# Kernel tuning notes

Hardware: AMD Instinct MI355X
Metric: run time of the kernel (lower is better)

The kernel has to match this reference:

```python
import jax, jax.numpy as jnp
import numpy as np

IMG, P, INC = 384, 2, 3
C = 2 * IMG            # embed_dim = 768
NP_ = IMG // P         # 192 patches
N = NP_ + 1            # 193 tokens with cls
L, H, E, K, B = 6, 12, 8, 2, 32
HD = C // H
EPS = 1e-5


def layer_norm(x, w, b):
    m = jnp.mean(x, -1, keepdims=True)
    v = jnp.mean((x - m) ** 2, -1, keepdims=True)
    return (x - m) * jax.lax.rsqrt(v + EPS) * w + b


def setup_inputs() -> dict:
    key = jax.random.key(0)
    ks = iter(jax.random.split(key, 32))
    nrm = lambda sh, s=0.02: jax.random.normal(next(ks), sh, jnp.float32) * s
    inp = {
        'x1': nrm((B, INC, IMG, IMG), 1.0),
        'x2': nrm((B, INC, IMG, IMG), 1.0),
        'patch_w': nrm((C, INC, IMG, P)),
        'patch_b': jnp.zeros((C,)),
        'cls_token': nrm((1, 1, C), 1e-6),
        'ln1_w': jnp.ones((L, C)), 'ln1_b': jnp.zeros((L, C)),
        'qkv_w': nrm((L, 3 * C, C)), 'qkv_b': jnp.zeros((L, 3 * C)),
        'proj_w': nrm((L, C, C)), 'proj_b': jnp.zeros((L, C)),
        'ln2_w': jnp.ones((L, C)), 'ln2_b': jnp.zeros((L, C)),
        'route_w': nrm((L, E, C)), 'route_b': jnp.zeros((L, E)),
        'rln_w': jnp.ones((L, E)), 'rln_b': jnp.zeros((L, E)),
        'expert_w': nrm((L, E, C, C)), 'expert_b': jnp.zeros((L, E, C)),
        'norm_w': jnp.ones((C,)), 'norm_b': jnp.zeros((C,)),
    }
    # fixed 1D sin-cos positional embedding (build_sincos_encoding)
    pd = C // 2
    omega = jnp.exp(jnp.arange(pd, dtype=jnp.float32) * (-np.log(10000.0) / pd))
    ow = jnp.arange(NP_, dtype=jnp.float32)[:, None] * omega
    pe = jnp.concatenate([jnp.sin(ow), jnp.cos(ow)], axis=1)          # [192, C]
    inp['pos_emb'] = jnp.concatenate([jnp.zeros((1, C)), pe], axis=0)[None]  # [1, N, C]
    return inp


def _patch_embed(x, patch_w, patch_b, cls_token, pos_emb):
    b = x.shape[0]
    # non-overlapping (IMG, P) conv == matmul on patches, flattened in (c, kh, kw) order
    xp = x.reshape(b, INC, IMG, NP_, P).transpose(0, 3, 1, 2, 4).reshape(b, NP_, INC * IMG * P)
    tok = xp @ patch_w.reshape(C, -1).T + patch_b                     # [B, 192, C]
    tok = jnp.concatenate([jnp.broadcast_to(cls_token, (b, 1, C)), tok], axis=1)
    return tok + pos_emb


def _encoder(x, view_id, ln1_w, ln1_b, qkv_w, qkv_b, proj_w, proj_b,
             ln2_w, ln2_b, route_w, route_b, rln_w, rln_b, expert_w, expert_b):
    scale = HD ** -0.5
    base = jax.random.fold_in(jax.random.key(1234), view_id)
    b = x.shape[0]

    def step(h, p):
        idx, l1w, l1b, qw, qb, pw, pb, l2w, l2b, rw, rb, rlw, rlb, ew, eb = p
        # --- attention ---
        y = layer_norm(h, l1w, l1b)
        qkv = (y @ qw.T + qb).reshape(b, N, 3, H, HD).transpose(2, 0, 3, 1, 4)
        q, k, v = qkv[0], qkv[1], qkv[2]
        a = jax.nn.softmax(jnp.einsum('bhqd,bhkd->bhqk', q, k) * scale, axis=-1)
        o = jnp.einsum('bhqk,bhkd->bhqd', a, v).transpose(0, 2, 1, 3).reshape(b, N, C)
        h = h + o @ pw.T + pb
        # --- MoE ---
        y = layer_norm(h, l2w, l2b)
        logits = layer_norm(y @ rw.T + rb, rlw, rlb)                  # [B, N, E]
        noise = jax.random.normal(jax.random.fold_in(base, idx), logits.shape) / E
        rwts = jax.nn.softmax(logits, axis=-1) + noise
        topw, topi = jax.lax.top_k(rwts, K)
        topw = jax.nn.softmax(topw, axis=-1)
        # dense all-expert compute, as in the source module
        eo = jnp.einsum('bni,eoi->bneo', y, ew) + eb                  # [B, N, E, C]
        sel = jnp.take_along_axis(eo, topi[..., None], axis=2)        # [B, N, K, C]
        h = h + (sel * topw[..., None]).sum(axis=2)
        return h, None

    xs = (jnp.arange(L), ln1_w, ln1_b, qkv_w, qkv_b, proj_w, proj_b,
          ln2_w, ln2_b, route_w, route_b, rln_w, rln_b, expert_w, expert_b)
    x, _ = jax.lax.scan(step, x, xs)
    return x


def reference(x1, x2, patch_w, patch_b, cls_token, ln1_w, ln1_b, qkv_w, qkv_b,
              proj_w, proj_b, ln2_w, ln2_b, route_w, route_b, rln_w, rln_b,
              expert_w, expert_b, norm_w, norm_b, pos_emb):
    def tower(x, vid):
        h = _patch_embed(x, patch_w, patch_b, cls_token, pos_emb)
        h = _encoder(h, vid, ln1_w, ln1_b, qkv_w, qkv_b, proj_w, proj_b,
                     ln2_w, ln2_b, route_w, route_b, rln_w, rln_b, expert_w, expert_b)
        return layer_norm(h, norm_w, norm_b)[:, 0]
    return jnp.concatenate([tower(x1, 0), tower(x2, 1)], axis=1)      # [B, 2*C]
```

## Files before the change

kernel.cpp:

```cpp
#include <hip/hip_runtime.h>
#include <stdint.h>

#define C_DIM   768
#define N_TOK   193
#define B_TOT   64
#define ROWS    (B_TOT * N_TOK)
#define QKV_DIM 2304
#define N_HEAD  12
#define N_EXP   8
#define MAXPER  ROWS
#define RTOK    64

enum { MODE_PATCH = 0, MODE_PLAIN = 1, MODE_RESID = 2, MODE_EXPERT = 3 };

typedef __attribute__((ext_vector_type(8))) short bf16x8;
typedef __attribute__((ext_vector_type(4))) float f32x4;

__device__ __forceinline__ uint32_t rotl32(uint32_t x, int n){ return (x << n) | (x >> (32 - n)); }

__device__ __forceinline__ void tf2x32(uint32_t k0, uint32_t k1, uint32_t x0, uint32_t x1,
                                       uint32_t &r0, uint32_t &r1){
  uint32_t k2 = k0 ^ k1 ^ 0x1BD11BDAu;
#define TF4(a,b,c,d) x0+=x1; x1=rotl32(x1,a); x1^=x0; x0+=x1; x1=rotl32(x1,b); x1^=x0; \
                     x0+=x1; x1=rotl32(x1,c); x1^=x0; x0+=x1; x1=rotl32(x1,d); x1^=x0;
  x0 += k0; x1 += k1;
  TF4(13,15,26, 6)  x0 += k1; x1 += k2 + 1u;
  TF4(17,29,16,24)  x0 += k2; x1 += k0 + 2u;
  TF4(13,15,26, 6)  x0 += k0; x1 += k1 + 3u;
  TF4(17,29,16,24)  x0 += k1; x1 += k2 + 4u;
  TF4(13,15,26, 6)  x0 += k2; x1 += k0 + 5u;
#undef TF4
  r0 = x0; r1 = x1;
}

__device__ __forceinline__ float jax_erfinv(float x){
  float w = -log1pf(-x * x);
  float p;
  if (w < 5.0f){
    w -= 2.5f;
    p =              2.81022636e-08f;
    p = fmaf(p, w,   3.43273939e-07f);
    p = fmaf(p, w,  -3.5233877e-06f);
    p = fmaf(p, w,  -4.39150654e-06f);
    p = fmaf(p, w,   0.00021858087f);
    p = fmaf(p, w,  -0.00125372503f);
    p = fmaf(p, w,  -0.00417768164f);
    p = fmaf(p, w,   0.246640727f);
    p = fmaf(p, w,   1.50140941f);
  } else {
    w = sqrtf(w) - 3.0f;
    p =             -0.000200214257f;
    p = fmaf(p, w,   0.000100950558f);
    p = fmaf(p, w,   0.00134934322f);
    p = fmaf(p, w,  -0.00367342844f);
    p = fmaf(p, w,   0.00573950773f);
    p = fmaf(p, w,  -0.0076224613f);
    p = fmaf(p, w,   0.00943887047f);
    p = fmaf(p, w,   1.00167406f);
    p = fmaf(p, w,   2.83297682f);
  }
  return p * x;
}

__device__ __forceinline__ float jax_noise(uint32_t c0, uint32_t c1, uint32_t j){
  uint32_t o0, o1;
  tf2x32(c0, c1, 0u, j, o0, o1);
  uint32_t bits = o0 ^ o1;
  float f = __uint_as_float(0x3f800000u | (bits >> 9)) - 1.0f;
  const float lo = -0.99999994f;
  float u = fmaxf(lo, f * 2.0f + lo);
  return 1.41421356237f * jax_erfinv(u) * 0.125f;
}

__device__ __forceinline__ unsigned short f2bf(float x){
  union { float f; uint32_t u; } v; v.f = x;
  uint32_t u = v.u;
  uint32_t r = (u + 0x7FFFu + ((u >> 16) & 1u)) >> 16;
  return (unsigned short)r;
}
__device__ __forceinline__ float bf2f(unsigned short h){
  union { uint32_t u; float f; } v; v.u = ((uint32_t)h) << 16;
  return v.f;
}

__global__ __launch_bounds__(64) void k_zero8(int* __restrict__ p){
  if ((int)threadIdx.x < N_EXP) p[threadIdx.x] = 0;
}

__global__ __launch_bounds__(64) void k_sentinel(float* __restrict__ out, float v){
  if (threadIdx.x == 0) out[0] = v;
}

__global__ __launch_bounds__(256) void k_cls(float* __restrict__ h, const float* __restrict__ cls,
                                             const float* __restrict__ pos){
  const int bt = blockIdx.x;
  #pragma unroll
  for (int u = 0; u < 3; ++u){
    int c = threadIdx.x + u * 256;
    h[(size_t)bt * N_TOK * C_DIM + c] = cls[c] + pos[c];
  }
}

__device__ __forceinline__ float blk_sum(float v, float* sb){
  #pragma unroll
  for (int off = 32; off > 0; off >>= 1) v += __shfl_down(v, off, 64);
  const int lane = threadIdx.x & 63, w = threadIdx.x >> 6;
  if (lane == 0) sb[w] = v;
  __syncthreads();
  if (threadIdx.x == 0) sb[4] = sb[0] + sb[1] + sb[2] + sb[3];
  __syncthreads();
  float r = sb[4];
  __syncthreads();
  return r;
}

__global__ __launch_bounds__(256) void k_layernorm(const float* __restrict__ x, float* __restrict__ y,
                                                   const float* __restrict__ w, const float* __restrict__ b){
  __shared__ float sb[8];
  const float* xr = x + (size_t)blockIdx.x * C_DIM;
  float v0 = xr[threadIdx.x], v1 = xr[threadIdx.x + 256], v2 = xr[threadIdx.x + 512];
  float mean = blk_sum(v0 + v1 + v2, sb) * (1.0f / 768.0f);
  float d0 = v0 - mean, d1 = v1 - mean, d2 = v2 - mean;
  float var = blk_sum(d0 * d0 + d1 * d1 + d2 * d2, sb) * (1.0f / 768.0f);
  float inv = 1.0f / sqrtf(var + 1e-5f);
  float* yr = y + (size_t)blockIdx.x * C_DIM;
  yr[threadIdx.x]       = d0 * inv * w[threadIdx.x]       + b[threadIdx.x];
  yr[threadIdx.x + 256] = d1 * inv * w[threadIdx.x + 256] + b[threadIdx.x + 256];
  yr[threadIdx.x + 512] = d2 * inv * w[threadIdx.x + 512] + b[threadIdx.x + 512];
}

__global__ __launch_bounds__(256) void k_final(const float* __restrict__ h, float* __restrict__ out,
                                               const float* __restrict__ w, const float* __restrict__ b){
  __shared__ float sb[8];
  const int bt = blockIdx.x;
  const float* xr = h + (size_t)bt * N_TOK * C_DIM;
  float v0 = xr[threadIdx.x], v1 = xr[threadIdx.x + 256], v2 = xr[threadIdx.x + 512];
  float mean = blk_sum(v0 + v1 + v2, sb) * (1.0f / 768.0f);
  float d0 = v0 - mean, d1 = v1 - mean, d2 = v2 - mean;
  float var = blk_sum(d0 * d0 + d1 * d1 + d2 * d2, sb) * (1.0f / 768.0f);
  float inv = 1.0f / sqrtf(var + 1e-5f);
  float* orow = out + (size_t)(bt & 31) * 1536 + (size_t)(bt >> 5) * C_DIM;
  orow[threadIdx.x]       = d0 * inv * w[threadIdx.x]       + b[threadIdx.x];
  orow[threadIdx.x + 256] = d1 * inv * w[threadIdx.x + 256] + b[threadIdx.x + 256];
  orow[threadIdx.x + 512] = d2 * inv * w[threadIdx.x + 512] + b[threadIdx.x + 512];
}

template<int MODE>
__global__ __launch_bounds__(256) void k_mgemm(
    const float* __restrict__ A, const float* __restrict__ W,
    const float* __restrict__ bias, float* __restrict__ C,
    int M, int Nc, int Kc,
    const float* __restrict__ xa, const float* __restrict__ xb,
    const float* __restrict__ pos,
    const int* __restrict__ elist, const int* __restrict__ ecnt)
{
  __shared__ short sAhi[128][40];
  __shared__ short sAlo[128][40];
  __shared__ short sBhi[128][40];
  __shared__ short sBlo[128][40];

  const int tid = threadIdx.x;

  int e = 0;
  int Mloc = M;
  const float* Wp = W;
  const float* bp = bias;
  if constexpr (MODE == MODE_EXPERT){
    e = blockIdx.z;
    Mloc = ecnt[e];
    Wp = W + (size_t)e * C_DIM * C_DIM;
    bp = bias + e * C_DIM;
  }
  const int row0 = blockIdx.x * 128;
  const int col0 = blockIdx.y * 128;
  if (row0 >= Mloc) return;

  const int srow = tid >> 1;
  const int skh  = (tid & 1) * 16;

  const float* arow = A;
  bool avalid = false;
  const float* psrc = nullptr;
  if constexpr (MODE == MODE_PLAIN || MODE == MODE_RESID){
    int r = row0 + srow;
    avalid = r < Mloc;
    arow = A + (size_t)(avalid ? r : 0) * Kc;
  } else if constexpr (MODE == MODE_EXPERT){
    int r = row0 + srow;
    avalid = r < Mloc;
    if (avalid) arow = A + (size_t)(elist[e * MAXPER + r] >> 1) * C_DIM;
  } else {
    int r = row0 + srow;
    int bt = r / 192;
    int n  = r - bt * 192;
    const float* xp = (bt < 32) ? xa : xb;
    psrc = xp + (size_t)(bt & 31) * 3 * 384 * 384 + n * 2;
    avalid = true;
  }
  const float* brow = Wp + (size_t)(col0 + srow) * Kc;

  const int wv = tid >> 6;
  const int wr = (wv >> 1) * 64;
  const int wc = (wv & 1) * 64;
  const int lane = tid & 63;
  const int lrow = lane & 15;
  const int lkh  = (lane >> 4) * 8;

  f32x4 acc[4][4] = {};

  const int nkt = Kc / 32;
  for (int kt = 0; kt < nkt; ++kt){
    const int k0 = kt * 32 + skh;
    {
      float va[16] = {};
      if constexpr (MODE == MODE_PATCH){
        int c   = k0 / 768;
        int rem = k0 - c * 768;
        const float* pc = psrc + ((size_t)c * 384 + (rem >> 1)) * 384;
        #pragma unroll
        for (int m = 0; m < 8; ++m){
          va[m * 2 + 0] = pc[(size_t)m * 384 + 0];
          va[m * 2 + 1] = pc[(size_t)m * 384 + 1];
        }
      } else {
        if (avalid){
          *(float4*)&va[0]  = *(const float4*)(arow + k0);
          *(float4*)&va[4]  = *(const float4*)(arow + k0 + 4);
          *(float4*)&va[8]  = *(const float4*)(arow + k0 + 8);
          *(float4*)&va[12] = *(const float4*)(arow + k0 + 12);
        }
      }
      short hi[16], lo[16];
      #pragma unroll
      for (int j = 0; j < 16; ++j){
        unsigned short hb = f2bf(va[j]);
        hi[j] = (short)hb;
        lo[j] = (short)f2bf(va[j] - bf2f(hb));
      }
      *(bf16x8*)&sAhi[srow][skh]     = *(bf16x8*)&hi[0];
      *(bf16x8*)&sAhi[srow][skh + 8] = *(bf16x8*)&hi[8];
      *(bf16x8*)&sAlo[srow][skh]     = *(bf16x8*)&lo[0];
      *(bf16x8*)&sAlo[srow][skh + 8] = *(bf16x8*)&lo[8];
    }
    {
      float vb[16];
      *(float4*)&vb[0]  = *(const float4*)(brow + k0);
      *(float4*)&vb[4]  = *(const float4*)(brow + k0 + 4);
      *(float4*)&vb[8]  = *(const float4*)(brow + k0 + 8);
      *(float4*)&vb[12] = *(const float4*)(brow + k0 + 12);
      short hi[16], lo[16];
      #pragma unroll
      for (int j = 0; j < 16; ++j){
        unsigned short hb = f2bf(vb[j]);
        hi[j] = (short)hb;
        lo[j] = (short)f2bf(vb[j] - bf2f(hb));
      }
      *(bf16x8*)&sBhi[srow][skh]     = *(bf16x8*)&hi[0];
      *(bf16x8*)&sBhi[srow][skh + 8] = *(bf16x8*)&hi[8];
      *(bf16x8*)&sBlo[srow][skh]     = *(bf16x8*)&lo[0];
      *(bf16x8*)&sBlo[srow][skh + 8] = *(bf16x8*)&lo[8];
    }
    __syncthreads();
    bf16x8 ahi[4], alo[4], bhi[4], blo[4];
    #pragma unroll
    for (int i = 0; i < 4; ++i){
      ahi[i] = *(const bf16x8*)&sAhi[wr + i * 16 + lrow][lkh];
      alo[i] = *(const bf16x8*)&sAlo[wr + i * 16 + lrow][lkh];
    }
    #pragma unroll
    for (int j = 0; j < 4; ++j){
      bhi[j] = *(const bf16x8*)&sBhi[wc + j * 16 + lrow][lkh];
      blo[j] = *(const bf16x8*)&sBlo[wc + j * 16 + lrow][lkh];
    }
    #pragma unroll
    for (int i = 0; i < 4; ++i)
      #pragma unroll
      for (int j = 0; j < 4; ++j){
        acc[i][j] = __builtin_amdgcn_mfma_f32_16x16x32_bf16(ahi[i], bhi[j], acc[i][j], 0, 0, 0);
        acc[i][j] = __builtin_amdgcn_mfma_f32_16x16x32_bf16(ahi[i], blo[j], acc[i][j], 0, 0, 0);
        acc[i][j] = __builtin_amdgcn_mfma_f32_16x16x32_bf16(alo[i], bhi[j], acc[i][j], 0, 0, 0);
      }
    __syncthreads();
  }

  #pragma unroll
  for (int i = 0; i < 4; ++i){
    const int rbase = row0 + wr + i * 16 + (lane >> 4) * 4;
    #pragma unroll
    for (int r = 0; r < 4; ++r){
      const int rg = rbase + r;
      if (rg >= Mloc) continue;
      if constexpr (MODE == MODE_PATCH){
        int bt = rg / 192, n = rg - (rg / 192) * 192;
        size_t orow = ((size_t)bt * N_TOK + n + 1) * C_DIM;
        size_t prow = (size_t)(n + 1) * C_DIM;
        #pragma unroll
        for (int j = 0; j < 4; ++j){
          int cg = col0 + wc + j * 16 + (lane & 15);
          C[orow + cg] = acc[i][j][r] + bp[cg] + pos[prow + cg];
        }
      } else if constexpr (MODE == MODE_PLAIN){
        size_t orow = (size_t)rg * Nc;
        #pragma unroll
        for (int j = 0; j < 4; ++j){
          int cg = col0 + wc + j * 16 + (lane & 15);
          C[orow + cg] = acc[i][j][r] + bp[cg];
        }
      } else if constexpr (MODE == MODE_RESID){
        size_t orow = (size_t)rg * Nc;
        #pragma unroll
        for (int j = 0; j < 4; ++j){
          int cg = col0 + wc + j * 16 + (lane & 15);
          C[orow + cg] += acc[i][j][r] + bp[cg];
        }
      } else {
        int ts = elist[e * MAXPER + rg];
        size_t orow = (size_t)ts * C_DIM;
        #pragma unroll
        for (int j = 0; j < 4; ++j){
          int cg = col0 + wc + j * 16 + (lane & 15);
          C[orow + cg] = acc[i][j][r] + bp[cg];
        }
      }
    }
  }
}

__global__ __launch_bounds__(256) void k_attn(const float* __restrict__ qkv, float* __restrict__ o_out){
  __shared__ short sQhi[64][72],  sQlo[64][72];
  __shared__ short sKPhi[64][72], sKPlo[64][72];
  __shared__ short sVThi[64][72], sVTlo[64][72];

  const int q0 = blockIdx.x * 64;
  const int bh = blockIdx.y;
  const int bt = bh / N_HEAD, hh = bh - bt * N_HEAD;
  const int tid = threadIdx.x;
  const size_t base = (size_t)bt * N_TOK * QKV_DIM + (size_t)hh * 64;

  const int srow = tid >> 2;
  const int sk   = (tid & 3) * 16;

  {
    float v[16] = {};
    int q = q0 + srow;
    if (q < N_TOK){
      const float* src = qkv + base + (size_t)q * QKV_DIM + sk;
      *(float4*)&v[0]  = *(const float4*)(src);
      *(float4*)&v[4]  = *(const float4*)(src + 4);
      *(float4*)&v[8]  = *(const float4*)(src + 8);
      *(float4*)&v[12] = *(const float4*)(src + 12);
    }
    short hi[16], lo[16];
    #pragma unroll
    for (int j = 0; j < 16; ++j){
      unsigned short hb = f2bf(v[j]);
      hi[j] = (short)hb;
      lo[j] = (short)f2bf(v[j] - bf2f(hb));
    }
    *(bf16x8*)&sQhi[srow][sk]     = *(bf16x8*)&hi[0];
    *(bf16x8*)&sQhi[srow][sk + 8] = *(bf16x8*)&hi[8];
    *(bf16x8*)&sQlo[srow][sk]     = *(bf16x8*)&lo[0];
    *(bf16x8*)&sQlo[srow][sk + 8] = *(bf16x8*)&lo[8];
  }

  const int wv   = tid >> 6;
  const int lane = tid & 63;
  const int lrow = lane & 15;
  const int lkh  = (lane >> 4) * 8;

  f32x4 Oacc[4] = {};
  float mrun[4] = {-1e30f, -1e30f, -1e30f, -1e30f};
  float lrun[4] = {};

  for (int kt = 0; kt < 4; ++kt){
    const int n0 = kt * 64;
    __syncthreads();
    {
      float v[16] = {};
      int kk = n0 + srow;
      bool valid = kk < N_TOK;
      if (valid){
        const float* src = qkv + base + 768 + (size_t)kk * QKV_DIM + sk;
        *(float4*)&v[0]  = *(const float4*)(src);
        *(float4*)&v[4]  = *(const float4*)(src + 4);
        *(float4*)&v[8]  = *(const float4*)(src + 8);
        *(float4*)&v[12] = *(const float4*)(src + 12);
      }
      short hi[16], lo[16];
      #pragma unroll
      for (int j = 0; j < 16; ++j){
        unsigned short hb = f2bf(v[j]);
        hi[j] = (short)hb;
        lo[j] = (short)f2bf(v[j] - bf2f(hb));
      }
      *(bf16x8*)&sKPhi[srow][sk]     = *(bf16x8*)&hi[0];
      *(bf16x8*)&sKPhi[srow][sk + 8] = *(bf16x8*)&hi[8];
      *(bf16x8*)&sKPlo[srow][sk]     = *(bf16x8*)&lo[0];
      *(bf16x8*)&sKPlo[srow][sk + 8] = *(bf16x8*)&lo[8];
      float vv[16] = {};
      if (valid){
        const float* src = qkv + base + 1536 + (size_t)kk * QKV_DIM + sk;
        *(float4*)&vv[0]  = *(const float4*)(src);
        *(float4*)&vv[4]  = *(const float4*)(src + 4);
        *(float4*)&vv[8]  = *(const float4*)(src + 8);
        *(float4*)&vv[12] = *(const float4*)(src + 12);
      }
      #pragma unroll
      for (int j = 0; j < 16; ++j){
        unsigned short hb = f2bf(vv[j]);
        sVThi[sk + j][srow] = (short)hb;
        sVTlo[sk + j][srow] = (short)f2bf(vv[j] - bf2f(hb));
      }
    }
    __syncthreads();

    f32x4 s[4] = {};
    {
      bf16x8 ahi0 = *(const bf16x8*)&sQhi[wv * 16 + lrow][lkh];
      bf16x8 alo0 = *(const bf16x8*)&sQlo[wv * 16 + lrow][lkh];
      bf16x8 ahi1 = *(const bf16x8*)&sQhi[wv * 16 + lrow][32 + lkh];
      bf16x8 alo1 = *(const bf16x8*)&sQlo[wv * 16 + lrow][32 + lkh];
      #pragma unroll
      for (int j = 0; j < 4; ++j){
        bf16x8 bhi0 = *(const bf16x8*)&sKPhi[j * 16 + lrow][lkh];
        bf16x8 blo0 = *(const bf16x8*)&sKPlo[j * 16 + lrow][lkh];
        bf16x8 bhi1 = *(const bf16x8*)&sKPhi[j * 16 + lrow][32 + lkh];
        bf16x8 blo1 = *(const bf16x8*)&sKPlo[j * 16 + lrow][32 + lkh];
        s[j] = __builtin_amdgcn_mfma_f32_16x16x32_bf16(ahi0, bhi0, s[j], 0, 0, 0);
        s[j] = __builtin_amdgcn_mfma_f32_16x16x32_bf16(ahi0, blo0, s[j], 0, 0, 0);
        s[j] = __builtin_amdgcn_mfma_f32_16x16x32_bf16(alo0, bhi0, s[j], 0, 0, 0);
        s[j] = __builtin_amdgcn_mfma_f32_16x16x32_bf16(ahi1, bhi1, s[j], 0, 0, 0);
        s[j] = __builtin_amdgcn_mfma_f32_16x16x32_bf16(ahi1, blo1, s[j], 0, 0, 0);
        s[j] = __builtin_amdgcn_mfma_f32_16x16x32_bf16(alo1, bhi1, s[j], 0, 0, 0);
      }
    }
    #pragma unroll
    for (int j = 0; j < 4; ++j){
      bool masked = (n0 + j * 16 + lrow) >= N_TOK;
      #pragma unroll
      for (int r = 0; r < 4; ++r){
        s[j][r] *= 0.125f;
        if (masked) s[j][r] = -1e30f;
      }
    }

    float p[4][4], fac[4];
    #pragma unroll
    for (int r = 0; r < 4; ++r){
      float rm = fmaxf(fmaxf(s[0][r], s[1][r]), fmaxf(s[2][r], s[3][r]));
      rm = fmaxf(rm, __shfl_xor(rm, 1, 64));
      rm = fmaxf(rm, __shfl_xor(rm, 2, 64));
      rm = fmaxf(rm, __shfl_xor(rm, 4, 64));
      rm = fmaxf(rm, __shfl_xor(rm, 8, 64));
      float mn = fmaxf(mrun[r], rm);
      fac[r] = expf(mrun[r] - mn);
      mrun[r] = mn;
      lrun[r] *= fac[r];
      float rs = 0.f;
      #pragma unroll
      for (int j = 0; j < 4; ++j){ p[j][r] = expf(s[j][r] - mn); rs += p[j][r]; }
      rs += __shfl_xor(rs, 1, 64);
      rs += __shfl_xor(rs, 2, 64);
      rs += __shfl_xor(rs, 4, 64);
      rs += __shfl_xor(rs, 8, 64);
      lrun[r] += rs;
      #pragma unroll
      for (int j = 0; j < 4; ++j) Oacc[j][r] *= fac[r];
    }

    __syncthreads();
    #pragma unroll
    for (int r = 0; r < 4; ++r){
      const int prow = wv * 16 + (lane >> 4) * 4 + r;
      #pragma unroll
      for (int j = 0; j < 4; ++j){
        unsigned short hb = f2bf(p[j][r]);
        sKPhi[prow][j * 16 + lrow] = (short)hb;
        sKPlo[prow][j * 16 + lrow] = (short)f2bf(p[j][r] - bf2f(hb));
      }
    }

    {
      bf16x8 phi0 = *(const bf16x8*)&sKPhi[wv * 16 + lrow][lkh];
      bf16x8 plo0 = *(const bf16x8*)&sKPlo[wv * 16 + lrow][lkh];
      bf16x8 phi1 = *(const bf16x8*)&sKPhi[wv * 16 + lrow][32 + lkh];
      bf16x8 plo1 = *(const bf16x8*)&sKPlo[wv * 16 + lrow][32 + lkh];
      #pragma unroll
      for (int j = 0; j < 4; ++j){
        bf16x8 vhi0 = *(const bf16x8*)&sVThi[j * 16 + lrow][lkh];
        bf16x8 vlo0 = *(const bf16x8*)&sVTlo[j * 16 + lrow][lkh];
        bf16x8 vhi1 = *(const bf16x8*)&sVThi[j * 16 + lrow][32 + lkh];
        bf16x8 vlo1 = *(const bf16x8*)&sVTlo[j * 16 + lrow][32 + lkh];
        Oacc[j] = __builtin_amdgcn_mfma_f32_16x16x32_bf16(phi0, vhi0, Oacc[j], 0, 0, 0);
        Oacc[j] = __builtin_amdgcn_mfma_f32_16x16x32_bf16(phi0, vlo0, Oacc[j], 0, 0, 0);
        Oacc[j] = __builtin_amdgcn_mfma_f32_16x16x32_bf16(plo0, vhi0, Oacc[j], 0, 0, 0);
        Oacc[j] = __builtin_amdgcn_mfma_f32_16x16x32_bf16(phi1, vhi1, Oacc[j], 0, 0, 0);
        Oacc[j] = __builtin_amdgcn_mfma_f32_16x16x32_bf16(phi1, vlo1, Oacc[j], 0, 0, 0);
        Oacc[j] = __builtin_amdgcn_mfma_f32_16x16x32_bf16(plo1, vhi1, Oacc[j], 0, 0, 0);
      }
    }
  }

  #pragma unroll
  for (int r = 0; r < 4; ++r){
    int q = q0 + wv * 16 + (lane >> 4) * 4 + r;
    if (q < N_TOK){
      float inv = 1.0f / lrun[r];
      #pragma unroll
      for (int j = 0; j < 4; ++j)
        o_out[((size_t)bt * N_TOK + q) * C_DIM + hh * 64 + j * 16 + lrow] = Oacc[j][r] * inv;
    }
  }
}

__global__ __launch_bounds__(256) void k_router(
    const float* __restrict__ y, const float* __restrict__ rw, const float* __restrict__ rb,
    const float* __restrict__ rlw, const float* __restrict__ rlb,
    float* __restrict__ topw, int* __restrict__ elist, int* __restrict__ ecnt, int l)
{
  __shared__ float4 sw4[1536];
  __shared__ int lcnt[8];
  __shared__ int lbase[8];
  __shared__ int llist[8][RTOK];
  const int tid = threadIdx.x;
  const float4* rw4 = (const float4*)rw;
  #pragma unroll
  for (int u = 0; u < 6; ++u)
    sw4[tid + u * 256] = rw4[tid + u * 256];
  if (tid < 8) lcnt[tid] = 0;
  __syncthreads();

  const int wid = tid >> 6, lane = tid & 63;
  const int e = lane & 7;

  for (int t16 = 0; t16 < RTOK / 4; ++t16){
    const int tok = blockIdx.x * RTOK + wid * (RTOK / 4) + t16;
    const float4* y4 = (const float4*)(y + (size_t)tok * C_DIM);
    const float4 a0 = y4[lane], a1 = y4[64 + lane], a2 = y4[128 + lane];

    float part[8];
    #pragma unroll
    for (int ee = 0; ee < 8; ++ee){
      const float4 w0 = sw4[ee * 192 + lane];
      const float4 w1 = sw4[ee * 192 + 64 + lane];
      const float4 w2 = sw4[ee * 192 + 128 + lane];
      float s = a0.x * w0.x;
      s = fmaf(a0.y, w0.y, s); s = fmaf(a0.z, w0.z, s); s = fmaf(a0.w, w0.w, s);
      s = fmaf(a1.x, w1.x, s); s = fmaf(a1.y, w1.y, s); s = fmaf(a1.z, w1.z, s); s = fmaf(a1.w, w1.w, s);
      s = fmaf(a2.x, w2.x, s); s = fmaf(a2.y, w2.y, s); s = fmaf(a2.z, w2.z, s); s = fmaf(a2.w, w2.w, s);
      part[ee] = s;
    }
    #pragma unroll
    for (int ee = 0; ee < 8; ++ee)
      #pragma unroll
      for (int off = 32; off; off >>= 1) part[ee] += __shfl_xor(part[ee], off, 64);

    float logit = part[e] + rb[e];
    float ssum = logit;
    ssum += __shfl_xor(ssum, 1, 64); ssum += __shfl_xor(ssum, 2, 64); ssum += __shfl_xor(ssum, 4, 64);
    float mean = ssum * 0.125f;
    float d = logit - mean;
    float vs = d * d;
    vs += __shfl_xor(vs, 1, 64); vs += __shfl_xor(vs, 2, 64); vs += __shfl_xor(vs, 4, 64);
    float ln = d * (1.0f / sqrtf(vs * 0.125f + 1e-5f)) * rlw[e] + rlb[e];
    float mx = ln;
    mx = fmaxf(mx, __shfl_xor(mx, 1, 64)); mx = fmaxf(mx, __shfl_xor(mx, 2, 64)); mx = fmaxf(mx, __shfl_xor(mx, 4, 64));
    float ex = expf(ln - mx);
    float es = ex;
    es += __shfl_xor(es, 1, 64); es += __shfl_xor(es, 2, 64); es += __shfl_xor(es, 4, 64);
    float prob = ex / es;
    int t = tok / 6176;
    int rem = tok - t * 6176;
    int b = rem / N_TOK, n = rem - (rem / N_TOK) * N_TOK;
    uint32_t b0, b1, c0, c1;
    tf2x32(0u, 1234u, 0u, (uint32_t)t, b0, b1);
    tf2x32(b0, b1, 0u, (uint32_t)l, c0, c1);
    uint32_t j = (uint32_t)(b * N_TOK + n) * 8u + (uint32_t)e;
    float r = prob + jax_noise(c0, c1, j);
    float v1 = r; int i1 = e;
    #pragma unroll
    for (int off = 1; off <= 4; off <<= 1){
      float ov = __shfl_xor(v1, off, 64); int oi = __shfl_xor(i1, off, 64);
      if (ov > v1 || (ov == v1 && oi < i1)){ v1 = ov; i1 = oi; }
    }
    float rm2 = (e == i1) ? -3.0e38f : r;
    float v2 = rm2; int i2 = e;
    #pragma unroll
    for (int off = 1; off <= 4; off <<= 1){
      float ov = __shfl_xor(v2, off, 64); int oi = __shfl_xor(i2, off, 64);
      if (ov > v2 || (ov == v2 && oi < i2)){ v2 = ov; i2 = oi; }
    }
    float e2 = expf(v2 - v1);
    float sum = 1.0f + e2;
    if (lane == 0){
      topw[tok * 2 + 0] = 1.0f / sum;
      topw[tok * 2 + 1] = e2 / sum;
      int p = atomicAdd(&lcnt[i1], 1);
      llist[i1][p] = tok * 2;
      int p2 = atomicAdd(&lcnt[i2], 1);
      llist[i2][p2] = tok * 2 + 1;
    }
  }
  __syncthreads();
  if (tid < 8) lbase[tid] = atomicAdd(&ecnt[tid], lcnt[tid]);
  __syncthreads();
  #pragma unroll
  for (int ee = 0; ee < 8; ++ee){
    const int cnt = lcnt[ee];
    const int bse = lbase[ee];
    for (int i = tid; i < cnt; i += 256)
      elist[ee * MAXPER + bse + i] = llist[ee][i];
  }
}

__global__ __launch_bounds__(256) void k_combine(float* __restrict__ h, const float* __restrict__ eout,
                                                 const float* __restrict__ topw){
  const int tok = blockIdx.x;
  const float w0 = topw[tok * 2], w1 = topw[tok * 2 + 1];
  const size_t hb = (size_t)tok * C_DIM;
  const size_t e0 = (size_t)(tok * 2) * C_DIM, e1 = e0 + C_DIM;
  #pragma unroll
  for (int u = 0; u < 3; ++u){
    int c = threadIdx.x + u * 256;
    h[hb + c] += w0 * eout[e0 + c] + w1 * eout[e1 + c];
  }
}

extern "C" void kernel_launch(void* const* d_in, const int* in_sizes, int n_in,
                              void* d_out, int out_size, void* d_ws, size_t ws_size,
                              hipStream_t stream){
  float* out = (float*)d_out;

  static const int kExp[22] = {
    14155776, 14155776, 1769472, 768, 768,
    4608, 4608, 10616832, 13824, 3538944, 4608,
    4608, 4608, 36864, 48, 48, 48,
    28311552, 36864, 768, 768, 148224};
  const size_t need_f = (size_t)ROWS * C_DIM * 2 + (size_t)ROWS * QKV_DIM
                      + (size_t)ROWS * 2 + (size_t)N_EXP * MAXPER + 8;
  float bad = 0.f;
  if (n_in != 22) bad = 2.0e6f;
  else {
    for (int i = 0; i < 22; ++i)
      if (in_sizes[i] != kExp[i]){ bad = 4.0e6f + i * 1.0e4f; break; }
  }
  if (bad == 0.f && out_size != 49152) bad = 3.0e6f;
  if (bad == 0.f && ws_size < need_f * 4) bad = 1.0e6f;
  if (bad != 0.f){
    k_sentinel<<<dim3(1), 64, 0, stream>>>(out, bad);
    return;
  }

  const float* x1       = (const float*)d_in[0];
  const float* x2       = (const float*)d_in[1];
  const float* patch_w  = (const float*)d_in[2];
  const float* patch_b  = (const float*)d_in[3];
  const float* cls_tok  = (const float*)d_in[4];
  const float* ln1_w    = (const float*)d_in[5];
  const float* ln1_b    = (const float*)d_in[6];
  const float* qkv_w    = (const float*)d_in[7];
  const float* qkv_b    = (const float*)d_in[8];
  const float* proj_w   = (const float*)d_in[9];
  const float* proj_b   = (const float*)d_in[10];
  const float* ln2_w    = (const float*)d_in[11];
  const float* ln2_b    = (const float*)d_in[12];
  const float* route_w  = (const float*)d_in[13];
  const float* route_b  = (const float*)d_in[14];
  const float* rln_w    = (const float*)d_in[15];
  const float* rln_b    = (const float*)d_in[16];
  const float* expert_w = (const float*)d_in[17];
  const float* expert_b = (const float*)d_in[18];
  const float* norm_w   = (const float*)d_in[19];
  const float* norm_b   = (const float*)d_in[20];
  const float* pos_emb  = (const float*)d_in[21];

  float* ws = (float*)d_ws;
  size_t off = 0;
  float* h    = ws + off; off += (size_t)ROWS * C_DIM;
  float* y    = ws + off; off += (size_t)ROWS * C_DIM;
  float* qkv  = ws + off; off += (size_t)ROWS * QKV_DIM;
  float* eout = qkv;
  float* topw = ws + off; off += (size_t)ROWS * 2;
  int*   elist = (int*)(ws + off); off += (size_t)N_EXP * MAXPER;
  int*   ecnt  = (int*)(ws + off); off += 8;

  k_cls<<<dim3(B_TOT), 256, 0, stream>>>(h, cls_tok, pos_emb);
  k_mgemm<MODE_PATCH><<<dim3(96, 6), 256, 0, stream>>>(
      nullptr, patch_w, patch_b, h, 12288, C_DIM, 2304, x1, x2, pos_emb, nullptr, nullptr);

  for (int l = 0; l < 6; ++l){
    k_layernorm<<<dim3(ROWS), 256, 0, stream>>>(h, y, ln1_w + l * C_DIM, ln1_b + l * C_DIM);
    k_mgemm<MODE_PLAIN><<<dim3(97, 18), 256, 0, stream>>>(
        y, qkv_w + (size_t)l * QKV_DIM * C_DIM, qkv_b + l * QKV_DIM, qkv,
        ROWS, QKV_DIM, C_DIM, nullptr, nullptr, nullptr, nullptr, nullptr);
    k_attn<<<dim3(4, B_TOT * N_HEAD), 256, 0, stream>>>(qkv, y);
    k_mgemm<MODE_RESID><<<dim3(97, 6), 256, 0, stream>>>(
        y, proj_w + (size_t)l * C_DIM * C_DIM, proj_b + l * C_DIM, h,
        ROWS, C_DIM, C_DIM, nullptr, nullptr, nullptr, nullptr, nullptr);
    k_layernorm<<<dim3(ROWS), 256, 0, stream>>>(h, y, ln2_w + l * C_DIM, ln2_b + l * C_DIM);
    k_zero8<<<dim3(1), 64, 0, stream>>>(ecnt);
    k_router<<<dim3(ROWS / RTOK), 256, 0, stream>>>(
        y, route_w + (size_t)l * N_EXP * C_DIM, route_b + l * N_EXP,
        rln_w + l * N_EXP, rln_b + l * N_EXP, topw, elist, ecnt, l);
    k_mgemm<MODE_EXPERT><<<dim3(97, 6, N_EXP), 256, 0, stream>>>(
        y, expert_w + (size_t)l * N_EXP * C_DIM * C_DIM, expert_b + (size_t)l * N_EXP * C_DIM, eout,
        ROWS, C_DIM, C_DIM, nullptr, nullptr, nullptr, elist, ecnt);
    k_combine<<<dim3(ROWS), 256, 0, stream>>>(h, eout, topw);
  }
  k_final<<<dim3(B_TOT), 256, 0, stream>>>(h, out, norm_w, norm_b);
}
```

Before: 4.072 ms.

## Pre-split activations and weights into bf16 hi/lo planes outside GEMM loops

Weights are converted once per layer into bf16 hi/lo arrays by a new split kernel. The layernorm and attention epilogues now also emit bf16 hi/lo copies of their outputs. The GEMM then loads pre-split shorts straight into shared memory instead of converting fp32 tiles on every k-step. This removes the repeated split arithmetic that every tile recomputed, at the cost of extra split-kernel launches, extra workspace and extra global writes of the split copies.

```diff
diff --git a/kernel.cpp b/kernel.cpp
--- a/kernel.cpp
+++ b/kernel.cpp
@@ -14,6 +14,7 @@
 enum { MODE_PATCH = 0, MODE_PLAIN = 1, MODE_RESID = 2, MODE_EXPERT = 3 };
 
 typedef __attribute__((ext_vector_type(8))) short bf16x8;
+typedef __attribute__((ext_vector_type(4))) short short4v;
 typedef __attribute__((ext_vector_type(4))) float f32x4;
 
 __device__ __forceinline__ uint32_t rotl32(uint32_t x, int n){ return (x << n) | (x >> (32 - n)); }
@@ -82,6 +83,11 @@
   union { uint32_t u; float f; } v; v.u = ((uint32_t)h) << 16;
   return v.f;
 }
+__device__ __forceinline__ void fsplit(float x, short &hi, short &lo){
+  unsigned short hb = f2bf(x);
+  hi = (short)hb;
+  lo = (short)f2bf(x - bf2f(hb));
+}
 
 __global__ __launch_bounds__(64) void k_zero8(int* __restrict__ p){
   if ((int)threadIdx.x < N_EXP) p[threadIdx.x] = 0;
@@ -89,6 +95,23 @@
 
 __global__ __launch_bounds__(64) void k_sentinel(float* __restrict__ out, float v){
   if (threadIdx.x == 0) out[0] = v;
+}
+
+__global__ __launch_bounds__(256) void k_wsplit(const float* __restrict__ w,
+                                                short* __restrict__ whi, short* __restrict__ wlo, int n4){
+  for (int i = blockIdx.x * 256 + threadIdx.x; i < n4; i += gridDim.x * 256){
+    float4 v = ((const float4*)w)[i];
+    short hx, lx, hy, ly, hz, lz, hw, lw;
+    fsplit(v.x, hx, lx);
+    fsplit(v.y, hy, ly);
+    fsplit(v.z, hz, lz);
+    fsplit(v.w, hw, lw);
+    short4v h, l;
+    h.x = hx; h.y = hy; h.z = hz; h.w = hw;
+    l.x = lx; l.y = ly; l.z = lz; l.w = lw;
+    ((short4v*)whi)[i] = h;
+    ((short4v*)wlo)[i] = l;
+  }
 }
 
 __global__ __launch_bounds__(256) void k_cls(float* __restrict__ h, const float* __restrict__ cls,
@@ -115,18 +138,27 @@
 }
 
 __global__ __launch_bounds__(256) void k_layernorm(const float* __restrict__ x, float* __restrict__ y,
+                                                   short* __restrict__ yhi, short* __restrict__ ylo,
                                                    const float* __restrict__ w, const float* __restrict__ b){
   __shared__ float sb[8];
-  const float* xr = x + (size_t)blockIdx.x * C_DIM;
+  const size_t rb = (size_t)blockIdx.x * C_DIM;
+  const float* xr = x + rb;
   float v0 = xr[threadIdx.x], v1 = xr[threadIdx.x + 256], v2 = xr[threadIdx.x + 512];
   float mean = blk_sum(v0 + v1 + v2, sb) * (1.0f / 768.0f);
   float d0 = v0 - mean, d1 = v1 - mean, d2 = v2 - mean;
   float var = blk_sum(d0 * d0 + d1 * d1 + d2 * d2, sb) * (1.0f / 768.0f);
   float inv = 1.0f / sqrtf(var + 1e-5f);
-  float* yr = y + (size_t)blockIdx.x * C_DIM;
-  yr[threadIdx.x]       = d0 * inv * w[threadIdx.x]       + b[threadIdx.x];
-  yr[threadIdx.x + 256] = d1 * inv * w[threadIdx.x + 256] + b[threadIdx.x + 256];
-  yr[threadIdx.x + 512] = d2 * inv * w[threadIdx.x + 512] + b[threadIdx.x + 512];
+  float o0 = d0 * inv * w[threadIdx.x]       + b[threadIdx.x];
+  float o1 = d1 * inv * w[threadIdx.x + 256] + b[threadIdx.x + 256];
+  float o2 = d2 * inv * w[threadIdx.x + 512] + b[threadIdx.x + 512];
+  y[rb + threadIdx.x]       = o0;
+  y[rb + threadIdx.x + 256] = o1;
+  y[rb + threadIdx.x + 512] = o2;
+  short h0, l0, h1, l1, h2, l2;
+  fsplit(o0, h0, l0); fsplit(o1, h1, l1); fsplit(o2, h2, l2);
+  yhi[rb + threadIdx.x]       = h0; ylo[rb + threadIdx.x]       = l0;
+  yhi[rb + threadIdx.x + 256] = h1; ylo[rb + threadIdx.x + 256] = l1;
+  yhi[rb + threadIdx.x + 512] = h2; ylo[rb + threadIdx.x + 512] = l2;
 }
 
 __global__ __launch_bounds__(256) void k_final(const float* __restrict__ h, float* __restrict__ out,
@@ -147,7 +179,8 @@
 
 template<int MODE>
 __global__ __launch_bounds__(256) void k_mgemm(
-    const float* __restrict__ A, const float* __restrict__ W,
+    const short* __restrict__ Ahi, const short* __restrict__ Alo,
+    const short* __restrict__ Whi, const short* __restrict__ Wlo,
     const float* __restrict__ bias, float* __restrict__ C,
     int M, int Nc, int Kc,
     const float* __restrict__ xa, const float* __restrict__ xb,
@@ -163,12 +196,14 @@
 
   int e = 0;
   int Mloc = M;
-  const float* Wp = W;
+  const short* Wph = Whi;
+  const short* Wpl = Wlo;
   const float* bp = bias;
   if constexpr (MODE == MODE_EXPERT){
     e = blockIdx.z;
     Mloc = ecnt[e];
-    Wp = W + (size_t)e * C_DIM * C_DIM;
+    Wph = Whi + (size_t)e * C_DIM * C_DIM;
+    Wpl = Wlo + (size_t)e * C_DIM * C_DIM;
     bp = bias + e * C_DIM;
   }
   const int row0 = blockIdx.x * 128;
@@ -178,17 +213,23 @@
   const int srow = tid >> 1;
   const int skh  = (tid & 1) * 16;
 
-  const float* arow = A;
+  const short* arowh = Ahi;
+  const short* arowl = Alo;
   bool avalid = false;
   const float* psrc = nullptr;
   if constexpr (MODE == MODE_PLAIN || MODE == MODE_RESID){
     int r = row0 + srow;
     avalid = r < Mloc;
-    arow = A + (size_t)(avalid ? r : 0) * Kc;
+    arowh = Ahi + (size_t)(avalid ? r : 0) * Kc;
+    arowl = Alo + (size_t)(avalid ? r : 0) * Kc;
   } else if constexpr (MODE == MODE_EXPERT){
     int r = row0 + srow;
     avalid = r < Mloc;
-    if (avalid) arow = A + (size_t)(elist[e * MAXPER + r] >> 1) * C_DIM;
+    if (avalid){
+      size_t ar = (size_t)(elist[e * MAXPER + r] >> 1) * C_DIM;
+      arowh = Ahi + ar;
+      arowl = Alo + ar;
+    }
   } else {
     int r = row0 + srow;
     int bt = r / 192;
@@ -197,7 +238,8 @@
     psrc = xp + (size_t)(bt & 31) * 3 * 384 * 384 + n * 2;
     avalid = true;
   }
-  const float* brow = Wp + (size_t)(col0 + srow) * Kc;
+  const short* browh = Wph + (size_t)(col0 + srow) * Kc;
+  const short* browl = Wpl + (size_t)(col0 + srow) * Kc;
 
   const int wv = tid >> 6;
   const int wr = (wv >> 1) * 64;
@@ -211,55 +253,41 @@
   const int nkt = Kc / 32;
   for (int kt = 0; kt < nkt; ++kt){
     const int k0 = kt * 32 + skh;
-    {
+    if constexpr (MODE == MODE_PATCH){
       float va[16] = {};
-      if constexpr (MODE == MODE_PATCH){
-        int c   = k0 / 768;
-        int rem = k0 - c * 768;
-        const float* pc = psrc + ((size_t)c * 384 + (rem >> 1)) * 384;
-        #pragma unroll
-        for (int m = 0; m < 8; ++m){
-          va[m * 2 + 0] = pc[(size_t)m * 384 + 0];
-          va[m * 2 + 1] = pc[(size_t)m * 384 + 1];
-        }
-      } else {
-        if (avalid){
-          *(float4*)&va[0]  = *(const float4*)(arow + k0);
-          *(float4*)&va[4]  = *(const float4*)(arow + k0 + 4);
-          *(float4*)&va[8]  = *(const float4*)(arow + k0 + 8);
-          *(float4*)&va[12] = *(const float4*)(arow + k0 + 12);
-        }
+      int c   = k0 / 768;
+      int rem = k0 - c * 768;
+      const float* pc = psrc + ((size_t)c * 384 + (rem >> 1)) * 384;
+      #pragma unroll
+      for (int m = 0; m < 8; ++m){
+        va[m * 2 + 0] = pc[(size_t)m * 384 + 0];
+        va[m * 2 + 1] = pc[(size_t)m * 384 + 1];
       }
       short hi[16], lo[16];
       #pragma unroll
-      for (int j = 0; j < 16; ++j){
-        unsigned short hb = f2bf(va[j]);
-        hi[j] = (short)hb;
-        lo[j] = (short)f2bf(va[j] - bf2f(hb));
-      }
+      for (int j = 0; j < 16; ++j) fsplit(va[j], hi[j], lo[j]);
       *(bf16x8*)&sAhi[srow][skh]     = *(bf16x8*)&hi[0];
       *(bf16x8*)&sAhi[srow][skh + 8] = *(bf16x8*)&hi[8];
       *(bf16x8*)&sAlo[srow][skh]     = *(bf16x8*)&lo[0];
       *(bf16x8*)&sAlo[srow][skh + 8] = *(bf16x8*)&lo[8];
-    }
-    {
-      float vb[16];
-      *(float4*)&vb[0]  = *(const float4*)(brow + k0);
-      *(float4*)&vb[4]  = *(const float4*)(brow + k0 + 4);
-      *(float4*)&vb[8]  = *(const float4*)(brow + k0 + 8);
-      *(float4*)&vb[12] = *(const float4*)(brow + k0 + 12);
-      short hi[16], lo[16];
-      #pragma unroll
-      for (int j = 0; j < 16; ++j){
-        unsigned short hb = f2bf(vb[j]);
-        hi[j] = (short)hb;
-        lo[j] = (short)f2bf(vb[j] - bf2f(hb));
-      }
-      *(bf16x8*)&sBhi[srow][skh]     = *(bf16x8*)&hi[0];
-      *(bf16x8*)&sBhi[srow][skh + 8] = *(bf16x8*)&hi[8];
-      *(bf16x8*)&sBlo[srow][skh]     = *(bf16x8*)&lo[0];
-      *(bf16x8*)&sBlo[srow][skh + 8] = *(bf16x8*)&lo[8];
-    }
+    } else {
+      if (avalid){
+        *(bf16x8*)&sAhi[srow][skh]     = *(const bf16x8*)(arowh + k0);
+        *(bf16x8*)&sAhi[srow][skh + 8] = *(const bf16x8*)(arowh + k0 + 8);
+        *(bf16x8*)&sAlo[srow][skh]     = *(const bf16x8*)(arowl + k0);
+        *(bf16x8*)&sAlo[srow][skh + 8] = *(const bf16x8*)(arowl + k0 + 8);
+      } else {
+        bf16x8 z = {0, 0, 0, 0, 0, 0, 0, 0};
+        *(bf16x8*)&sAhi[srow][skh]     = z;
+        *(bf16x8*)&sAhi[srow][skh + 8] = z;
+        *(bf16x8*)&sAlo[srow][skh]     = z;
+        *(bf16x8*)&sAlo[srow][skh + 8] = z;
+      }
+    }
+    *(bf16x8*)&sBhi[srow][skh]     = *(const bf16x8*)(browh + k0);
+    *(bf16x8*)&sBhi[srow][skh + 8] = *(const bf16x8*)(browh + k0 + 8);
+    *(bf16x8*)&sBlo[srow][skh]     = *(const bf16x8*)(browl + k0);
+    *(bf16x8*)&sBlo[srow][skh + 8] = *(const bf16x8*)(browl + k0 + 8);
     __syncthreads();
     bf16x8 ahi[4], alo[4], bhi[4], blo[4];
     #pragma unroll
@@ -326,7 +354,8 @@
   }
 }
 
-__global__ __launch_bounds__(256) void k_attn(const float* __restrict__ qkv, float* __restrict__ o_out){
+__global__ __launch_bounds__(256) void k_attn(const float* __restrict__ qkv, float* __restrict__ o_out,
+                                              short* __restrict__ ohi, short* __restrict__ olo){
   __shared__ short sQhi[64][72],  sQlo[64][72];
   __shared__ short sKPhi[64][72], sKPlo[64][72];
   __shared__ short sVThi[64][72], sVTlo[64][72];
@@ -352,11 +381,7 @@
     }
     short hi[16], lo[16];
     #pragma unroll
-    for (int j = 0; j < 16; ++j){
-      unsigned short hb = f2bf(v[j]);
-      hi[j] = (short)hb;
-      lo[j] = (short)f2bf(v[j] - bf2f(hb));
-    }
+    for (int j = 0; j < 16; ++j) fsplit(v[j], hi[j], lo[j]);
     *(bf16x8*)&sQhi[srow][sk]     = *(bf16x8*)&hi[0];
     *(bf16x8*)&sQhi[srow][sk + 8] = *(bf16x8*)&hi[8];
     *(bf16x8*)&sQlo[srow][sk]     = *(bf16x8*)&lo[0];
@@ -388,11 +413,7 @@
       }
       short hi[16], lo[16];
       #pragma unroll
-      for (int j = 0; j < 16; ++j){
-        unsigned short hb = f2bf(v[j]);
-        hi[j] = (short)hb;
-        lo[j] = (short)f2bf(v[j] - bf2f(hb));
-      }
+      for (int j = 0; j < 16; ++j) fsplit(v[j], hi[j], lo[j]);
       *(bf16x8*)&sKPhi[srow][sk]     = *(bf16x8*)&hi[0];
       *(bf16x8*)&sKPhi[srow][sk + 8] = *(bf16x8*)&hi[8];
       *(bf16x8*)&sKPlo[srow][sk]     = *(bf16x8*)&lo[0];
@@ -407,9 +428,10 @@
       }
       #pragma unroll
       for (int j = 0; j < 16; ++j){
-        unsigned short hb = f2bf(vv[j]);
-        sVThi[sk + j][srow] = (short)hb;
-        sVTlo[sk + j][srow] = (short)f2bf(vv[j] - bf2f(hb));
+        short h2, l2;
+        fsplit(vv[j], h2, l2);
+        sVThi[sk + j][srow] = h2;
+        sVTlo[sk + j][srow] = l2;
       }
     }
     __syncthreads();
@@ -474,9 +496,10 @@
       const int prow = wv * 16 + (lane >> 4) * 4 + r;
       #pragma unroll
       for (int j = 0; j < 4; ++j){
-        unsigned short hb = f2bf(p[j][r]);
-        sKPhi[prow][j * 16 + lrow] = (short)hb;
-        sKPlo[prow][j * 16 + lrow] = (short)f2bf(p[j][r] - bf2f(hb));
+        short h2, l2;
+        fsplit(p[j][r], h2, l2);
+        sKPhi[prow][j * 16 + lrow] = h2;
+        sKPlo[prow][j * 16 + lrow] = l2;
       }
     }
 
@@ -507,8 +530,15 @@
     if (q < N_TOK){
       float inv = 1.0f / lrun[r];
       #pragma unroll
-      for (int j = 0; j < 4; ++j)
-        o_out[((size_t)bt * N_TOK + q) * C_DIM + hh * 64 + j * 16 + lrow] = Oacc[j][r] * inv;
+      for (int j = 0; j < 4; ++j){
+        size_t idx = ((size_t)bt * N_TOK + q) * C_DIM + hh * 64 + j * 16 + lrow;
+        float val = Oacc[j][r] * inv;
+        o_out[idx] = val;
+        short h2, l2;
+        fsplit(val, h2, l2);
+        ohi[idx] = h2;
+        olo[idx] = l2;
+      }
     }
   }
 }
@@ -636,8 +666,12 @@
     4608, 4608, 10616832, 13824, 3538944, 4608,
     4608, 4608, 36864, 48, 48, 48,
     28311552, 36864, 768, 768, 148224};
-  const size_t need_f = (size_t)ROWS * C_DIM * 2 + (size_t)ROWS * QKV_DIM
-                      + (size_t)ROWS * 2 + (size_t)N_EXP * MAXPER + 8;
+  const size_t F_H    = (size_t)ROWS * C_DIM;
+  const size_t F_QKV  = (size_t)ROWS * QKV_DIM;
+  const size_t F_YSPL = ((size_t)ROWS * C_DIM + 1) / 2;
+  const size_t F_WB   = ((size_t)N_EXP * C_DIM * C_DIM + 1) / 2;
+  const size_t need_f = F_H * 2 + F_QKV + (size_t)ROWS * 2 + (size_t)N_EXP * MAXPER + 8
+                      + F_YSPL * 2 + F_WB * 2;
   float bad = 0.f;
   if (n_in != 22) bad = 2.0e6f;
   else {
@@ -676,34 +710,45 @@
 
   float* ws = (float*)d_ws;
   size_t off = 0;
-  float* h    = ws + off; off += (size_t)ROWS * C_DIM;
-  float* y    = ws + off; off += (size_t)ROWS * C_DIM;
-  float* qkv  = ws + off; off += (size_t)ROWS * QKV_DIM;
+  float* h    = ws + off; off += F_H;
+  float* y    = ws + off; off += F_H;
+  float* qkv  = ws + off; off += F_QKV;
   float* eout = qkv;
   float* topw = ws + off; off += (size_t)ROWS * 2;
   int*   elist = (int*)(ws + off); off += (size_t)N_EXP * MAXPER;
   int*   ecnt  = (int*)(ws + off); off += 8;
+  short* yhi  = (short*)(ws + off); off += F_YSPL;
+  short* ylo  = (short*)(ws + off); off += F_YSPL;
+  short* wbh  = (short*)(ws + off); off += F_WB;
+  short* wbl  = (short*)(ws + off); off += F_WB;
 
   k_cls<<<dim3(B_TOT), 256, 0, stream>>>(h, cls_tok, pos_emb);
+  k_wsplit<<<dim3(1024), 256, 0, stream>>>(patch_w, wbh, wbl, 1769472 / 4);
   k_mgemm<MODE_PATCH><<<dim3(96, 6), 256, 0, stream>>>(
-      nullptr, patch_w, patch_b, h, 12288, C_DIM, 2304, x1, x2, pos_emb, nullptr, nullptr);
+      nullptr, nullptr, wbh, wbl, patch_b, h, 12288, C_DIM, 2304, x1, x2, pos_emb, nullptr, nullptr);
 
   for (int l = 0; l < 6; ++l){
-    k_layernorm<<<dim3(ROWS), 256, 0, stream>>>(h, y, ln1_w + l * C_DIM, ln1_b + l * C_DIM);
+    k_layernorm<<<dim3(ROWS), 256, 0, stream>>>(h, y, yhi, ylo, ln1_w + l * C_DIM, ln1_b + l * C_DIM);
+    k_wsplit<<<dim3(1024), 256, 0, stream>>>(qkv_w + (size_t)l * QKV_DIM * C_DIM, wbh, wbl,
+                                             QKV_DIM * C_DIM / 4);
     k_mgemm<MODE_PLAIN><<<dim3(97, 18), 256, 0, stream>>>(
-        y, qkv_w + (size_t)l * QKV_DIM * C_DIM, qkv_b + l * QKV_DIM, qkv,
+        yhi, ylo, wbh, wbl, qkv_b + l * QKV_DIM, qkv,
         ROWS, QKV_DIM, C_DIM, nullptr, nullptr, nullptr, nullptr, nullptr);
-    k_attn<<<dim3(4, B_TOT * N_HEAD), 256, 0, stream>>>(qkv, y);
+    k_attn<<<dim3(4, B_TOT * N_HEAD), 256, 0, stream>>>(qkv, y, yhi, ylo);
+    k_wsplit<<<dim3(1024), 256, 0, stream>>>(proj_w + (size_t)l * C_DIM * C_DIM, wbh, wbl,
+                                             C_DIM * C_DIM / 4);
     k_mgemm<MODE_RESID><<<dim3(97, 6), 256, 0, stream>>>(
-        y, proj_w + (size_t)l * C_DIM * C_DIM, proj_b + l * C_DIM, h,
+        yhi, ylo, wbh, wbl, proj_b + l * C_DIM, h,
         ROWS, C_DIM, C_DIM, nullptr, nullptr, nullptr, nullptr, nullptr);
-    k_layernorm<<<dim3(ROWS), 256, 0, stream>>>(h, y, ln2_w + l * C_DIM, ln2_b + l * C_DIM);
+    k_layernorm<<<dim3(ROWS), 256, 0, stream>>>(h, y, yhi, ylo, ln2_w + l * C_DIM, ln2_b + l * C_DIM);
     k_zero8<<<dim3(1), 64, 0, stream>>>(ecnt);
     k_router<<<dim3(ROWS / RTOK), 256, 0, stream>>>(
         y, route_w + (size_t)l * N_EXP * C_DIM, route_b + l * N_EXP,
         rln_w + l * N_EXP, rln_b + l * N_EXP, topw, elist, ecnt, l);
+    k_wsplit<<<dim3(2048), 256, 0, stream>>>(expert_w + (size_t)l * N_EXP * C_DIM * C_DIM, wbh, wbl,
+                                             N_EXP * C_DIM * C_DIM / 4);
     k_mgemm<MODE_EXPERT><<<dim3(97, 6, N_EXP), 256, 0, stream>>>(
-        y, expert_w + (size_t)l * N_EXP * C_DIM * C_DIM, expert_b + (size_t)l * N_EXP * C_DIM, eout,
+        yhi, ylo, wbh, wbl, expert_b + (size_t)l * N_EXP * C_DIM, eout,
         ROWS, C_DIM, C_DIM, nullptr, nullptr, nullptr, elist, ecnt);
     k_combine<<<dim3(ROWS), 256, 0, stream>>>(h, eout, topw);
   }
```

New measurement: 5.789 ms. +42.2%, slower.

## Prefetch next GEMM K-tile into registers and fuse MoE combine with next LayerNorm

Applied to the files above, without the earlier changes.

The GEMM kernel now loads the next K-tile's A and B values from global memory into registers right after the barrier, so the loads overlap with the MFMA work on the current tile. Separately, the MoE combine step for layers 0-4 is fused with the following layer's LN1, which removes one read pass over the hidden state and one launch per layer. The price is higher register pressure in the GEMM, which may reduce occupancy.

```diff
diff --git a/kernel.cpp b/kernel.cpp
--- a/kernel.cpp
+++ b/kernel.cpp
@@ -129,6 +129,31 @@
   yr[threadIdx.x + 512] = d2 * inv * w[threadIdx.x + 512] + b[threadIdx.x + 512];
 }
 
+__global__ __launch_bounds__(256) void k_combine_ln(
+    float* __restrict__ h, const float* __restrict__ eout, const float* __restrict__ topw,
+    float* __restrict__ y, const float* __restrict__ w, const float* __restrict__ b)
+{
+  __shared__ float sb[8];
+  const int tok = blockIdx.x;
+  const float w0 = topw[tok * 2], w1 = topw[tok * 2 + 1];
+  const size_t hb = (size_t)tok * C_DIM;
+  const size_t e0 = (size_t)(tok * 2) * C_DIM, e1 = e0 + C_DIM;
+  const int t = threadIdx.x;
+  float v0 = h[hb + t]       + (w0 * eout[e0 + t]       + w1 * eout[e1 + t]);
+  float v1 = h[hb + t + 256] + (w0 * eout[e0 + t + 256] + w1 * eout[e1 + t + 256]);
+  float v2 = h[hb + t + 512] + (w0 * eout[e0 + t + 512] + w1 * eout[e1 + t + 512]);
+  h[hb + t]       = v0;
+  h[hb + t + 256] = v1;
+  h[hb + t + 512] = v2;
+  float mean = blk_sum(v0 + v1 + v2, sb) * (1.0f / 768.0f);
+  float d0 = v0 - mean, d1 = v1 - mean, d2 = v2 - mean;
+  float var = blk_sum(d0 * d0 + d1 * d1 + d2 * d2, sb) * (1.0f / 768.0f);
+  float inv = 1.0f / sqrtf(var + 1e-5f);
+  y[hb + t]       = d0 * inv * w[t]       + b[t];
+  y[hb + t + 256] = d1 * inv * w[t + 256] + b[t + 256];
+  y[hb + t + 512] = d2 * inv * w[t + 512] + b[t + 512];
+}
+
 __global__ __launch_bounds__(256) void k_final(const float* __restrict__ h, float* __restrict__ out,
                                                const float* __restrict__ w, const float* __restrict__ b){
   __shared__ float sb[8];
@@ -208,28 +233,42 @@
 
   f32x4 acc[4][4] = {};
 
+  float va[16], vb[16];
+  auto loadA = [&](int k0){
+    if constexpr (MODE == MODE_PATCH){
+      int c   = k0 / 768;
+      int rem = k0 - c * 768;
+      const float* pc = psrc + ((size_t)c * 384 + (rem >> 1)) * 384;
+      #pragma unroll
+      for (int m = 0; m < 8; ++m){
+        va[m * 2 + 0] = pc[(size_t)m * 384 + 0];
+        va[m * 2 + 1] = pc[(size_t)m * 384 + 1];
+      }
+    } else {
+      if (avalid){
+        *(float4*)&va[0]  = *(const float4*)(arow + k0);
+        *(float4*)&va[4]  = *(const float4*)(arow + k0 + 4);
+        *(float4*)&va[8]  = *(const float4*)(arow + k0 + 8);
+        *(float4*)&va[12] = *(const float4*)(arow + k0 + 12);
+      } else {
+        #pragma unroll
+        for (int j = 0; j < 16; ++j) va[j] = 0.f;
+      }
+    }
+  };
+  auto loadB = [&](int k0){
+    *(float4*)&vb[0]  = *(const float4*)(brow + k0);
+    *(float4*)&vb[4]  = *(const float4*)(brow + k0 + 4);
+    *(float4*)&vb[8]  = *(const float4*)(brow + k0 + 8);
+    *(float4*)&vb[12] = *(const float4*)(brow + k0 + 12);
+  };
+
+  loadA(skh);
+  loadB(skh);
+
   const int nkt = Kc / 32;
   for (int kt = 0; kt < nkt; ++kt){
-    const int k0 = kt * 32 + skh;
     {
-      float va[16] = {};
-      if constexpr (MODE == MODE_PATCH){
-        int c   = k0 / 768;
-        int rem = k0 - c * 768;
-        const float* pc = psrc + ((size_t)c * 384 + (rem >> 1)) * 384;
-        #pragma unroll
-        for (int m = 0; m < 8; ++m){
-          va[m * 2 + 0] = pc[(size_t)m * 384 + 0];
-          va[m * 2 + 1] = pc[(size_t)m * 384 + 1];
-        }
-      } else {
-        if (avalid){
-          *(float4*)&va[0]  = *(const float4*)(arow + k0);
-          *(float4*)&va[4]  = *(const float4*)(arow + k0 + 4);
-          *(float4*)&va[8]  = *(const float4*)(arow + k0 + 8);
-          *(float4*)&va[12] = *(const float4*)(arow + k0 + 12);
-        }
-      }
       short hi[16], lo[16];
       #pragma unroll
       for (int j = 0; j < 16; ++j){
@@ -241,14 +280,6 @@
       *(bf16x8*)&sAhi[srow][skh + 8] = *(bf16x8*)&hi[8];
       *(bf16x8*)&sAlo[srow][skh]     = *(bf16x8*)&lo[0];
       *(bf16x8*)&sAlo[srow][skh + 8] = *(bf16x8*)&lo[8];
-    }
-    {
-      float vb[16];
-      *(float4*)&vb[0]  = *(const float4*)(brow + k0);
-      *(float4*)&vb[4]  = *(const float4*)(brow + k0 + 4);
-      *(float4*)&vb[8]  = *(const float4*)(brow + k0 + 8);
-      *(float4*)&vb[12] = *(const float4*)(brow + k0 + 12);
-      short hi[16], lo[16];
       #pragma unroll
       for (int j = 0; j < 16; ++j){
         unsigned short hb = f2bf(vb[j]);
@@ -261,6 +292,10 @@
       *(bf16x8*)&sBlo[srow][skh + 8] = *(bf16x8*)&lo[8];
     }
     __syncthreads();
+    if (kt + 1 < nkt){
+      loadA((kt + 1) * 32 + skh);
+      loadB((kt + 1) * 32 + skh);
+    }
     bf16x8 ahi[4], alo[4], bhi[4], blo[4];
     #pragma unroll
     for (int i = 0; i < 4; ++i){
@@ -688,8 +723,8 @@
   k_mgemm<MODE_PATCH><<<dim3(96, 6), 256, 0, stream>>>(
       nullptr, patch_w, patch_b, h, 12288, C_DIM, 2304, x1, x2, pos_emb, nullptr, nullptr);
 
+  k_layernorm<<<dim3(ROWS), 256, 0, stream>>>(h, y, ln1_w, ln1_b);
   for (int l = 0; l < 6; ++l){
-    k_layernorm<<<dim3(ROWS), 256, 0, stream>>>(h, y, ln1_w + l * C_DIM, ln1_b + l * C_DIM);
     k_mgemm<MODE_PLAIN><<<dim3(97, 18), 256, 0, stream>>>(
         y, qkv_w + (size_t)l * QKV_DIM * C_DIM, qkv_b + l * QKV_DIM, qkv,
         ROWS, QKV_DIM, C_DIM, nullptr, nullptr, nullptr, nullptr, nullptr);
@@ -705,7 +740,12 @@
     k_mgemm<MODE_EXPERT><<<dim3(97, 6, N_EXP), 256, 0, stream>>>(
         y, expert_w + (size_t)l * N_EXP * C_DIM * C_DIM, expert_b + (size_t)l * N_EXP * C_DIM, eout,
         ROWS, C_DIM, C_DIM, nullptr, nullptr, nullptr, elist, ecnt);
-    k_combine<<<dim3(ROWS), 256, 0, stream>>>(h, eout, topw);
+    if (l < 5){
+      k_combine_ln<<<dim3(ROWS), 256, 0, stream>>>(
+          h, eout, topw, y, ln1_w + (l + 1) * C_DIM, ln1_b + (l + 1) * C_DIM);
+    } else {
+      k_combine<<<dim3(ROWS), 256, 0, stream>>>(h, eout, topw);
+    }
   }
   k_final<<<dim3(B_TOT), 256, 0, stream>>>(h, out, norm_w, norm_b);
 }
```

New measurement: 3.822 ms. -6.1%, faster.
